# Performance work log

Hardware: AMD Instinct MI355X
Metric: run time of the kernel (lower is better)

Reference implementation:

```python
import jax, jax.numpy as jnp
import numpy as np
import math

B, S, H = 8, 1024, 768
NH = 12
DH = H // NH


def _linear(x, W, b):
    # torch Linear: y = x @ W.T + b, W: [out, in]
    return jnp.einsum('bsd,ed->bse', x, W) + b


def _split_heads(x):
    # [B,S,H] -> [B,NH,S,DH]
    b, s, _ = x.shape
    return x.reshape(b, s, NH, DH).transpose(0, 2, 1, 3)


def _attend(q, k, v):
    # q,k,v: [B,NH,S,DH]
    scores = jnp.einsum('bhqd,bhkd->bhqk', q, k) / math.sqrt(DH)
    probs = jax.nn.softmax(scores, axis=-1)
    ctx = jnp.einsum('bhqk,bhkd->bhqd', probs, v)
    b, h, s, d = ctx.shape
    return ctx.transpose(0, 2, 1, 3).reshape(b, s, h * d)


def setup_inputs() -> dict:
    key = jax.random.key(0)
    ks = jax.random.split(key, 20)
    sc = 1.0 / math.sqrt(H)
    inp = {
        'hidden_statesx': jax.random.normal(ks[0], (B, S, H), jnp.float32),
        'hidden_statesy': jax.random.normal(ks[1], (B, S, H), jnp.float32),
    }
    names = ['Wq', 'Wk', 'Wv', 'Wo', 'Wqd', 'Wkd', 'Wvd', 'Wod']
    for i, n in enumerate(names):
        inp[n] = jax.random.normal(ks[2 + i], (H, H), jnp.float32) * sc
        inp['b' + n[1:]] = jnp.zeros((H,), jnp.float32)
    inp['w11'] = jnp.full((1,), 0.5, jnp.float32)
    inp['w12'] = jnp.full((1,), 0.5, jnp.float32)
    inp['w21'] = jnp.full((1,), 0.5, jnp.float32)
    inp['w22'] = jnp.full((1,), 0.5, jnp.float32)
    return inp


def reference(hidden_statesx, hidden_statesy,
              Wq, bq, Wk, bk, Wv, bv, Wo, bo,
              Wqd, bqd, Wkd, bkd, Wvd, bvd, Wod, bod,
              w11, w12, w21, w22):
    q = _split_heads(_linear(hidden_statesx, Wq, bq))
    k = _split_heads(_linear(hidden_statesx, Wk, bk))
    v = _split_heads(_linear(hidden_statesx, Wv, bv))
    qd = _split_heads(_linear(hidden_statesy, Wqd, bqd))
    kd = _split_heads(_linear(hidden_statesy, Wkd, bkd))
    vd = _split_heads(_linear(hidden_statesy, Wvd, bvd))

    # self-attention on x and y streams
    attention_sx = _linear(_attend(q, k, v), Wo, bo)
    attention_sy = _linear(_attend(qd, kd, vd), Wod, bod)
    # cross attentions (mba mode)
    attention_cx = _linear(_attend(q, kd, vd), Wo, bo)
    attention_cy = _linear(_attend(qd, k, v), Wod, bod)

    attention_sx = w11 * attention_sx + w12 * attention_cx
    attention_sy = w21 * attention_sy + w22 * attention_cy
    return attention_sx, attention_sy
```

## Files before the change

### kernel.cpp

```cpp
#include <hip/hip_runtime.h>

typedef __bf16 bf16;
typedef __bf16 bf16x8 __attribute__((ext_vector_type(8)));
typedef float f32x4 __attribute__((ext_vector_type(4)));

#define HD 768
#define ELTS 6291456
#define WELTS 589824

__device__ __forceinline__ void gld_lds16(const bf16* g, bf16* l) {
  __builtin_amdgcn_global_load_lds((const __attribute__((address_space(1))) void*)g,
                                   (__attribute__((address_space(3))) void*)l, 16, 0, 0);
}

__device__ __forceinline__ float rdscalar(const void* p, int f) {
  return f ? (float)((const bf16*)p)[0] : ((const float*)p)[0];
}

__device__ __forceinline__ float exp2fast(float x) {
#if __has_builtin(__builtin_amdgcn_exp2f)
  return __builtin_amdgcn_exp2f(x);
#else
  return __builtin_exp2f(x);
#endif
}

__global__ void probe_dtype(const unsigned int* __restrict__ x, int* flag) {
  const int t = threadIdx.x;
  int bad = 0;
#pragma unroll
  for (int i = 0; i < 4; ++i) {
    unsigned int wd = x[t * 4 + i];
    unsigned int e0 = (wd >> 7) & 0xFF;
    unsigned int e1 = (wd >> 23) & 0xFF;
    bad += (e0 >= 134) + (e1 >= 134);
  }
  unsigned long long m = __ballot(bad > 0);
  if (t == 0) *flag = (m == 0ULL) ? 1 : 0;
}

struct CvtArgs {
  const float* src[20];
  bf16* dst[20];
  int n[20];
  const int* flag;
};
__global__ __launch_bounds__(256) void convert_inputs(CvtArgs a) {
  if (*a.flag) return;
  const int seg = blockIdx.y;
  const float* s = a.src[seg];
  bf16* d = a.dst[seg];
  const int n4 = a.n[seg] >> 2;
  for (int i = blockIdx.x * blockDim.x + threadIdx.x; i < n4; i += gridDim.x * blockDim.x) {
    f32x4 v = *(const f32x4*)(s + i * 4);
    bf16 o[4];
#pragma unroll
    for (int e = 0; e < 4; ++e) o[e] = (bf16)v[e];
    *(unsigned long long*)(d + i * 4) = *(unsigned long long*)o;
  }
}

struct GemmArgs {
  const void* A[6];
  const void* Ac[6];
  const void* W[6];
  const void* Wc[6];
  const void* bias[6];
  const void* biasc[6];
  const void* s0[6];
  const void* s1[6];
  void* C[6];
  float cmul[6];
  int c_fixed[6];
  int vt[6];
  int ext_w[6];
  long long out_elem_off[6];
  const int* flag;
};

__global__ __launch_bounds__(256) void gemm_bt(GemmArgs args) {
  const int g = blockIdx.z;
  const int f = *args.flag;
  const bool c_bf = args.c_fixed[g] || f;
  const bool w_f32 = (!f) && args.ext_w[g];
  const bf16* __restrict__ A = (const bf16*)(f ? args.A[g] : args.Ac[g]);
  const void* __restrict__ Wp = f ? args.W[g] : args.Wc[g];
  const void* __restrict__ bias = f ? args.bias[g] : args.biasc[g];
  bf16* Cb = (bf16*)args.C[g] + args.out_elem_off[g];
  float* Cf = (float*)args.C[g] + args.out_elem_off[g];
  float bscale = 1.0f;
  if (args.s0[g]) bscale = rdscalar(args.s0[g], f) + rdscalar(args.s1[g], f);
  const float cmul = args.cmul[g];

  const int m0 = blockIdx.x * 128;
  const int n0 = blockIdx.y * 128;
  const int t = threadIdx.x;
  const int lane = t & 63;
  const int w = t >> 6;
  const int wm = (w >> 1) * 64, wn = (w & 1) * 64;

  __shared__ __attribute__((aligned(16))) bf16 As[128 * 64];
  __shared__ __attribute__((aligned(16))) bf16 Bs[128 * 64];

  f32x4 acc[4][4] = {};

  const int row_s = t >> 3, slot_s = t & 7;
  const int gswz = (slot_s ^ (row_s & 7)) << 3;

  const int fr = lane & 15;
  const int l4 = lane >> 4;
  const int sR0 = ((l4) ^ (fr & 7)) << 3;
  const int sR1 = ((4 + l4) ^ (fr & 7)) << 3;

  for (int kb = 0; kb < 12; ++kb) {
    const int k0 = kb * 64;
#pragma unroll
    for (int i = 0; i < 4; ++i) {
      const int row = row_s + i * 32;
      gld_lds16(A + (size_t)(m0 + row) * HD + k0 + gswz, As + (t + i * 256) * 8);
    }
    if (!w_f32) {
#pragma unroll
      for (int i = 0; i < 4; ++i) {
        const int row = row_s + i * 32;
        gld_lds16((const bf16*)Wp + (size_t)(n0 + row) * HD + k0 + gswz, Bs + (t + i * 256) * 8);
      }
    } else {
      const float* Wf = (const float*)Wp;
#pragma unroll
      for (int i = 0; i < 4; ++i) {
        const int row = row_s + i * 32;
        const size_t src = (size_t)(n0 + row) * HD + k0 + gswz;
        f32x4 u0 = *(const f32x4*)(Wf + src), u1 = *(const f32x4*)(Wf + src + 4);
        bf16x8 v;
#pragma unroll
        for (int e = 0; e < 4; ++e) { v[e] = (bf16)u0[e]; v[e + 4] = (bf16)u1[e]; }
        *(bf16x8*)(Bs + (t + i * 256) * 8) = v;
      }
    }
    __syncthreads();
#pragma unroll
    for (int kk = 0; kk < 2; ++kk) {
      const int sR = kk ? sR1 : sR0;
      bf16x8 af[4], bfr[4];
#pragma unroll
      for (int mi = 0; mi < 4; ++mi)
        af[mi] = *(const bf16x8*)(As + (wm + mi * 16 + fr) * 64 + sR);
#pragma unroll
      for (int ni = 0; ni < 4; ++ni)
        bfr[ni] = *(const bf16x8*)(Bs + (wn + ni * 16 + fr) * 64 + sR);
#pragma unroll
      for (int mi = 0; mi < 4; ++mi)
#pragma unroll
        for (int ni = 0; ni < 4; ++ni)
          acc[mi][ni] = __builtin_amdgcn_mfma_f32_16x16x32_bf16(af[mi], bfr[ni], acc[mi][ni], 0, 0, 0);
    }
    __syncthreads();
  }

  const int rq = (lane >> 4) * 4;
  const int is_vt = args.vt[g];
#pragma unroll
  for (int ni = 0; ni < 4; ++ni) {
    const int col = n0 + wn + ni * 16 + fr;
    const float bv = (w_f32 ? ((const float*)bias)[col]
                            : (float)((const bf16*)bias)[col]) * bscale;
#pragma unroll
    for (int mi = 0; mi < 4; ++mi) {
      const int row = m0 + wm + mi * 16 + rq;
      if (is_vt) {
        const int bb = row >> 10, s = row & 1023;
        const int hh = col >> 6, d = col & 63;
        bf16 tmp[4];
#pragma unroll
        for (int r = 0; r < 4; ++r) tmp[r] = (bf16)((acc[mi][ni][r] + bv) * cmul);
        *(unsigned long long*)(Cb + (((size_t)(bb * 12 + hh)) << 16) + (d << 10) + s) =
            *(const unsigned long long*)tmp;
      } else {
#pragma unroll
        for (int r = 0; r < 4; ++r) {
          const float val = (acc[mi][ni][r] + bv) * cmul;
          if (c_bf) Cb[(size_t)(row + r) * HD + col] = (bf16)val;
          else      Cf[(size_t)(row + r) * HD + col] = val;
        }
      }
    }
  }
}

__global__ __launch_bounds__(256, 2) void attn_mba(
    const bf16* __restrict__ Q, const bf16* __restrict__ Kx, const bf16* __restrict__ Vtx,
    const bf16* __restrict__ Qd, const bf16* __restrict__ Kd, const bf16* __restrict__ Vtd,
    const void* w11, const void* w12, const void* w21, const void* w22,
    bf16* ctxX, bf16* ctxY, const int* flag) {
  const int linear = blockIdx.x + (blockIdx.y << 4);
  const int swz = (linear & 7) * 192 + (linear >> 3);
  const int qb = swz & 15;
  const int bh = swz >> 4;
  const int b = bh / 12;
  const int f = *flag;

  const float wgtX[2] = {rdscalar(w11, f), rdscalar(w12, f)};
  const float wgtY[2] = {rdscalar(w22, f), rdscalar(w21, f)};

  const size_t tok0 = (size_t)b * 1024;
  const size_t vbase = (size_t)bh * 65536;
  const int fcol = (bh - b * 12) * 64;
  const int q0 = qb * 64;

  __shared__ __attribute__((aligned(16))) bf16 smem[16384];
  bf16* Ks = smem;
  bf16* Vs = smem + 8192;

  const int t = threadIdx.x, lane = t & 63, w = t >> 6;
  const int l15 = lane & 15, l4 = lane >> 4;

  const int g0 = t >> 3, slot0 = t & 7;
  const int g1 = g0 + 32;
  const int gs = (slot0 ^ (g0 & 7)) << 3;
  const int kp0 = (g0 & 32) + ((g0 & 12) << 1) + ((g0 & 16) >> 2) + (g0 & 3);
  const int kp1 = (g1 & 32) + ((g1 & 12) << 1) + ((g1 & 16) >> 2) + (g1 & 3);
  const size_t koffg0 = (tok0 + kp0) * HD + fcol + gs;
  const size_t koffg1 = (tok0 + kp1) * HD + fcol + gs;
  const size_t voffg0 = vbase + (size_t)g0 * 1024 + gs;
  const size_t voffg1 = vbase + (size_t)g1 * 1024 + gs;

  auto stage = [&](int nit) {
    const bf16* Kc = nit < 16 ? Kx : Kd;
    const bf16* Vc = nit < 16 ? Vtx : Vtd;
    const int kt64 = (nit & 15) * 64;
    bf16* Kb = Ks + (nit & 1) * 4096;
    bf16* Vb = Vs + (nit & 1) * 4096;
    gld_lds16(Kc + koffg0 + (size_t)kt64 * HD, Kb + t * 8);
    gld_lds16(Kc + koffg1 + (size_t)kt64 * HD, Kb + (t + 256) * 8);
    gld_lds16(Vc + voffg0 + kt64, Vb + t * 8);
    gld_lds16(Vc + voffg1 + kt64, Vb + (t + 256) * 8);
  };

  stage(0);

  const int qrow = w * 16 + l15;
  const bf16* qp0 = Q  + (tok0 + q0 + qrow) * HD + fcol;
  const bf16* qp1 = Qd + (tok0 + q0 + qrow) * HD + fcol;
  bf16x8 qf[2][2];
  qf[0][0] = *(const bf16x8*)(qp0 + (l4 << 3));
  qf[0][1] = *(const bf16x8*)(qp0 + ((4 + l4) << 3));
  qf[1][0] = *(const bf16x8*)(qp1 + (l4 << 3));
  qf[1][1] = *(const bf16x8*)(qp1 + ((4 + l4) << 3));

  const int kbase = l15 * 64 + ((l4 ^ (l15 & 7)) << 3);

  __syncthreads();

  f32x4 mixX[4] = {}, mixY[4] = {};
  f32x4 oacc[2][4] = {};
  f32x4 lsum[2] = {};

  for (int it = 0; it < 32; ++it) {
    if (it) __syncthreads();
    if (it + 1 < 32) stage(it + 1);
    const bf16* Kb = Ks + (it & 1) * 4096;
    const bf16* Vb = Vs + (it & 1) * 4096;

    const bf16* vpa = Vb + kbase;
    const bf16* vpb = Vb + (kbase ^ 32);
    const bf16x8 va0 = *(const bf16x8*)(vpa);
    const bf16x8 va1 = *(const bf16x8*)(vpa + 1024);
    const bf16x8 va2 = *(const bf16x8*)(vpa + 2048);
    const bf16x8 va3 = *(const bf16x8*)(vpa + 3072);
    const bf16x8 vb0 = *(const bf16x8*)(vpb);
    const bf16x8 vb1 = *(const bf16x8*)(vpb + 1024);
    const bf16x8 vb2 = *(const bf16x8*)(vpb + 2048);
    const bf16x8 vb3 = *(const bf16x8*)(vpb + 3072);

    f32x4 sv0[4], sv1[4];
    __builtin_amdgcn_s_setprio(1);
#pragma unroll
    for (int mi = 0; mi < 4; ++mi) {
      const bf16x8 kf0 = *(const bf16x8*)(Kb + (kbase + mi * 1024));
      const bf16x8 kf1 = *(const bf16x8*)(Kb + ((kbase ^ 32) + mi * 1024));
      f32x4 a = {}, c = {};
      a = __builtin_amdgcn_mfma_f32_16x16x32_bf16(kf0, qf[0][0], a, 0, 0, 0);
      c = __builtin_amdgcn_mfma_f32_16x16x32_bf16(kf0, qf[1][0], c, 0, 0, 0);
      a = __builtin_amdgcn_mfma_f32_16x16x32_bf16(kf1, qf[0][1], a, 0, 0, 0);
      c = __builtin_amdgcn_mfma_f32_16x16x32_bf16(kf1, qf[1][1], c, 0, 0, 0);
      sv0[mi] = a; sv1[mi] = c;
    }
    __builtin_amdgcn_s_setprio(0);

    bf16x8 pf00, pf01;
    {
      f32x4 ls = lsum[0];
#pragma unroll
      for (int mi = 0; mi < 4; ++mi) {
        f32x4 e;
#pragma unroll
        for (int r = 0; r < 4; ++r) e[r] = exp2fast(sv0[mi][r]);
        sv0[mi] = e;
        ls += e;
      }
      lsum[0] = ls;
#pragma unroll
      for (int j = 0; j < 8; ++j) {
        pf00[j] = (bf16)sv0[(j >> 2)][j & 3];
        pf01[j] = (bf16)sv0[2 + (j >> 2)][j & 3];
      }
    }
    bf16x8 pf10, pf11;
    {
      f32x4 ls = lsum[1];
#pragma unroll
      for (int mi = 0; mi < 4; ++mi) {
        f32x4 e;
#pragma unroll
        for (int r = 0; r < 4; ++r) e[r] = exp2fast(sv1[mi][r]);
        sv1[mi] = e;
        ls += e;
      }
      lsum[1] = ls;
#pragma unroll
      for (int j = 0; j < 8; ++j) {
        pf10[j] = (bf16)sv1[(j >> 2)][j & 3];
        pf11[j] = (bf16)sv1[2 + (j >> 2)][j & 3];
      }
    }

    __builtin_amdgcn_s_setprio(1);
    oacc[0][0] = __builtin_amdgcn_mfma_f32_16x16x32_bf16(va0, pf00, oacc[0][0], 0, 0, 0);
    oacc[1][0] = __builtin_amdgcn_mfma_f32_16x16x32_bf16(va0, pf10, oacc[1][0], 0, 0, 0);
    oacc[0][1] = __builtin_amdgcn_mfma_f32_16x16x32_bf16(va1, pf00, oacc[0][1], 0, 0, 0);
    oacc[1][1] = __builtin_amdgcn_mfma_f32_16x16x32_bf16(va1, pf10, oacc[1][1], 0, 0, 0);
    oacc[0][2] = __builtin_amdgcn_mfma_f32_16x16x32_bf16(va2, pf00, oacc[0][2], 0, 0, 0);
    oacc[1][2] = __builtin_amdgcn_mfma_f32_16x16x32_bf16(va2, pf10, oacc[1][2], 0, 0, 0);
    oacc[0][3] = __builtin_amdgcn_mfma_f32_16x16x32_bf16(va3, pf00, oacc[0][3], 0, 0, 0);
    oacc[1][3] = __builtin_amdgcn_mfma_f32_16x16x32_bf16(va3, pf10, oacc[1][3], 0, 0, 0);
    oacc[0][0] = __builtin_amdgcn_mfma_f32_16x16x32_bf16(vb0, pf01, oacc[0][0], 0, 0, 0);
    oacc[1][0] = __builtin_amdgcn_mfma_f32_16x16x32_bf16(vb0, pf11, oacc[1][0], 0, 0, 0);
    oacc[0][1] = __builtin_amdgcn_mfma_f32_16x16x32_bf16(vb1, pf01, oacc[0][1], 0, 0, 0);
    oacc[1][1] = __builtin_amdgcn_mfma_f32_16x16x32_bf16(vb1, pf11, oacc[1][1], 0, 0, 0);
    oacc[0][2] = __builtin_amdgcn_mfma_f32_16x16x32_bf16(vb2, pf01, oacc[0][2], 0, 0, 0);
    oacc[1][2] = __builtin_amdgcn_mfma_f32_16x16x32_bf16(vb2, pf11, oacc[1][2], 0, 0, 0);
    oacc[0][3] = __builtin_amdgcn_mfma_f32_16x16x32_bf16(vb3, pf01, oacc[0][3], 0, 0, 0);
    oacc[1][3] = __builtin_amdgcn_mfma_f32_16x16x32_bf16(vb3, pf11, oacc[1][3], 0, 0, 0);
    __builtin_amdgcn_s_setprio(0);

    if ((it & 15) == 15) {
      const int ph = it >> 4;
      float l0 = (lsum[0][0] + lsum[0][1]) + (lsum[0][2] + lsum[0][3]);
      float l1 = (lsum[1][0] + lsum[1][1]) + (lsum[1][2] + lsum[1][3]);
      l0 += __shfl_xor(l0, 16); l0 += __shfl_xor(l0, 32);
      l1 += __shfl_xor(l1, 16); l1 += __shfl_xor(l1, 32);
      const float scX = wgtX[ph] / l0;
      const float scY = wgtY[ph] / l1;
#pragma unroll
      for (int mi = 0; mi < 4; ++mi) {
#pragma unroll
        for (int r = 0; r < 4; ++r) {
          mixX[mi][r] += scX * oacc[0][mi][r];
          mixY[mi][r] += scY * oacc[1][mi][r];
        }
        oacc[0][mi] = f32x4{};
        oacc[1][mi] = f32x4{};
      }
      lsum[0] = f32x4{};
      lsum[1] = f32x4{};
    }
  }

  __syncthreads();
  bf16* TX = smem;
  bf16* TY = smem + 4608;
#pragma unroll
  for (int mi = 0; mi < 4; ++mi)
#pragma unroll
    for (int r = 0; r < 4; ++r) {
      TX[qrow * 72 + mi * 16 + l4 * 4 + r] = (bf16)mixX[mi][r];
      TY[qrow * 72 + mi * 16 + l4 * 4 + r] = (bf16)mixY[mi][r];
    }
  __syncthreads();
#pragma unroll
  for (int i = 0; i < 2; ++i) {
    const int q = t + i * 256;
    const int g = q >> 3, dc = (q & 7) * 8;
    *(bf16x8*)(ctxX + (tok0 + q0 + g) * HD + fcol + dc) = *(const bf16x8*)(TX + g * 72 + dc);
    *(bf16x8*)(ctxY + (tok0 + q0 + g) * HD + fcol + dc) = *(const bf16x8*)(TY + g * 72 + dc);
  }
}

extern "C" void kernel_launch(void* const* d_in, const int* in_sizes, int n_in,
                              void* d_out, int out_size, void* d_ws, size_t ws_size,
                              hipStream_t stream) {
  (void)in_sizes; (void)n_in; (void)out_size;
  const void* x = d_in[0];
  const void* y = d_in[1];

  bf16* ws = (bf16*)d_ws;
  bf16* Qb   = ws + 0ull * ELTS;
  bf16* Kb   = ws + 1ull * ELTS;
  bf16* Vtb  = ws + 2ull * ELTS;
  bf16* Qdb  = ws + 3ull * ELTS;
  bf16* Kdb  = ws + 4ull * ELTS;
  bf16* Vtdb = ws + 5ull * ELTS;
  bf16* ctxX = Qb;
  bf16* ctxY = Qdb;
  int* flag = (int*)(ws + 6ull * ELTS);

  const size_t extra_elems = 6ull * ELTS + 32 + 2ull * WELTS + 2 * 768;
  const bool big_ws = ws_size >= extra_elems * sizeof(bf16);
  bf16* extraW = ws + 6ull * ELTS + 32;
  bf16* extraB = extraW + 2ull * WELTS;

  bf16* cb = (bf16*)d_out;
  bf16* xb = cb;
  bf16* yb = cb + (size_t)ELTS;
  bf16* Wcv = cb + 2ull * ELTS;
  bf16* bcv = Wcv + 6ull * WELTS;

  probe_dtype<<<dim3(1), dim3(64), 0, stream>>>((const unsigned int*)x, flag);

  CvtArgs ca;
  int nseg = 14;
  {
    const int wsrc[6] = {2, 4, 6, 10, 12, 14};
    ca.src[0] = (const float*)x;  ca.dst[0] = xb;  ca.n[0] = ELTS;
    ca.src[1] = (const float*)y;  ca.dst[1] = yb;  ca.n[1] = ELTS;
    for (int i = 0; i < 6; ++i) {
      ca.src[2 + i] = (const float*)d_in[wsrc[i]];
      ca.dst[2 + i] = Wcv + (size_t)i * WELTS;
      ca.n[2 + i] = WELTS;
      ca.src[8 + i] = (const float*)d_in[wsrc[i] + 1];
      ca.dst[8 + i] = bcv + (size_t)i * 768;
      ca.n[8 + i] = 768;
    }
    if (big_ws) {
      ca.src[14] = (const float*)d_in[8];  ca.dst[14] = extraW;         ca.n[14] = WELTS;
      ca.src[15] = (const float*)d_in[16]; ca.dst[15] = extraW + WELTS; ca.n[15] = WELTS;
      ca.src[16] = (const float*)d_in[9];  ca.dst[16] = extraB;         ca.n[16] = 768;
      ca.src[17] = (const float*)d_in[17]; ca.dst[17] = extraB + 768;   ca.n[17] = 768;
      nseg = 18;
    }
    ca.flag = flag;
  }
  convert_inputs<<<dim3(512, nseg), dim3(256), 0, stream>>>(ca);

  GemmArgs gq;
  {
    const void* A6[6]  = {x, x, x, y, y, y};
    const void* Ac6[6] = {xb, xb, xb, yb, yb, yb};
    const int di[6] = {2, 4, 6, 10, 12, 14};
    bf16* C6[6] = {Qb, Kb, Vtb, Qdb, Kdb, Vtdb};
    for (int i = 0; i < 6; ++i) {
      gq.A[i] = A6[i]; gq.Ac[i] = Ac6[i];
      gq.W[i] = d_in[di[i]]; gq.Wc[i] = Wcv + (size_t)i * WELTS;
      gq.bias[i] = d_in[di[i] + 1]; gq.biasc[i] = bcv + (size_t)i * 768;
      gq.s0[i] = nullptr; gq.s1[i] = nullptr; gq.C[i] = C6[i];
      gq.cmul[i] = (i == 0 || i == 3) ? 0.18033688011112042f : 1.0f;
      gq.c_fixed[i] = 1; gq.ext_w[i] = 0; gq.out_elem_off[i] = 0;
      gq.vt[i] = (i == 2 || i == 5) ? 1 : 0;
    }
    gq.flag = flag;
  }
  gemm_bt<<<dim3(64, 6, 6), dim3(256), 0, stream>>>(gq);

  attn_mba<<<dim3(16, 96), dim3(256), 0, stream>>>(
      Qb, Kb, Vtb, Qdb, Kdb, Vtdb, d_in[18], d_in[19], d_in[20], d_in[21],
      ctxX, ctxY, flag);

  GemmArgs gp;
  for (int i = 0; i < 6; ++i) {
    gp.A[i] = ctxX; gp.Ac[i] = ctxX;
    gp.W[i] = d_in[8]; gp.Wc[i] = d_in[8];
    gp.bias[i] = d_in[9]; gp.biasc[i] = d_in[9];
    gp.s0[i] = d_in[18]; gp.s1[i] = d_in[19]; gp.C[i] = d_out;
    gp.cmul[i] = 1.0f; gp.c_fixed[i] = 0; gp.vt[i] = 0;
    gp.ext_w[i] = 1; gp.out_elem_off[i] = 0;
  }
  gp.A[1] = ctxY; gp.Ac[1] = ctxY;
  gp.W[1] = d_in[16]; gp.Wc[1] = d_in[16];
  gp.bias[1] = d_in[17]; gp.biasc[1] = d_in[17];
  gp.s0[1] = d_in[20]; gp.s1[1] = d_in[21];
  gp.out_elem_off[1] = (long long)ELTS;
  if (big_ws) {
    gp.Wc[0] = extraW;         gp.biasc[0] = extraB;       gp.ext_w[0] = 0;
    gp.Wc[1] = extraW + WELTS; gp.biasc[1] = extraB + 768; gp.ext_w[1] = 0;
  }
  gp.flag = flag;
  gemm_bt<<<dim3(64, 6, 2), dim3(256), 0, stream>>>(gp);
}
```

Measured before the change: 372.0 us.

## Double-buffer GEMM LDS tiles with K=32 to overlap loads and MFMA

Splits the projection GEMM's 64-wide K tile into two 32-wide LDS buffers and prefetches the next tile while MFMAs run on the current one. The swizzle is adapted to 4 slots per row. The goal is to hide global-to-LDS load latency behind compute while keeping total LDS use the same. In exchange there are twice as many K iterations, each with fewer MFMAs per barrier, so sync overhead relative to compute goes up.

```diff
diff --git a/kernel.cpp b/kernel.cpp
--- a/kernel.cpp
+++ b/kernel.cpp
@@ -99,63 +99,61 @@
   const int w = t >> 6;
   const int wm = (w >> 1) * 64, wn = (w & 1) * 64;
 
-  __shared__ __attribute__((aligned(16))) bf16 As[128 * 64];
-  __shared__ __attribute__((aligned(16))) bf16 Bs[128 * 64];
+  __shared__ __attribute__((aligned(16))) bf16 As[2][128 * 32];
+  __shared__ __attribute__((aligned(16))) bf16 Bs[2][128 * 32];
 
   f32x4 acc[4][4] = {};
 
-  const int row_s = t >> 3, slot_s = t & 7;
-  const int gswz = (slot_s ^ (row_s & 7)) << 3;
+  const int row_s = t >> 2;
+  const int gswz = (((t & 3) ^ (row_s & 3)) << 3);
 
   const int fr = lane & 15;
   const int l4 = lane >> 4;
-  const int sR0 = ((l4) ^ (fr & 7)) << 3;
-  const int sR1 = ((4 + l4) ^ (fr & 7)) << 3;
-
-  for (int kb = 0; kb < 12; ++kb) {
-    const int k0 = kb * 64;
-#pragma unroll
-    for (int i = 0; i < 4; ++i) {
-      const int row = row_s + i * 32;
-      gld_lds16(A + (size_t)(m0 + row) * HD + k0 + gswz, As + (t + i * 256) * 8);
-    }
+  const int sR = ((l4 ^ (fr & 3)) << 3);
+
+  auto stageAB = [&](int kb) {
+    const int buf = kb & 1;
+    const int k0 = kb * 32;
+    gld_lds16(A + (size_t)(m0 + row_s) * HD + k0 + gswz, &As[buf][t * 8]);
+    gld_lds16(A + (size_t)(m0 + row_s + 64) * HD + k0 + gswz, &As[buf][(t + 256) * 8]);
     if (!w_f32) {
-#pragma unroll
-      for (int i = 0; i < 4; ++i) {
-        const int row = row_s + i * 32;
-        gld_lds16((const bf16*)Wp + (size_t)(n0 + row) * HD + k0 + gswz, Bs + (t + i * 256) * 8);
-      }
+      gld_lds16((const bf16*)Wp + (size_t)(n0 + row_s) * HD + k0 + gswz, &Bs[buf][t * 8]);
+      gld_lds16((const bf16*)Wp + (size_t)(n0 + row_s + 64) * HD + k0 + gswz, &Bs[buf][(t + 256) * 8]);
     } else {
       const float* Wf = (const float*)Wp;
 #pragma unroll
-      for (int i = 0; i < 4; ++i) {
-        const int row = row_s + i * 32;
+      for (int i = 0; i < 2; ++i) {
+        const int row = row_s + i * 64;
         const size_t src = (size_t)(n0 + row) * HD + k0 + gswz;
         f32x4 u0 = *(const f32x4*)(Wf + src), u1 = *(const f32x4*)(Wf + src + 4);
         bf16x8 v;
 #pragma unroll
         for (int e = 0; e < 4; ++e) { v[e] = (bf16)u0[e]; v[e + 4] = (bf16)u1[e]; }
-        *(bf16x8*)(Bs + (t + i * 256) * 8) = v;
-      }
-    }
-    __syncthreads();
-#pragma unroll
-    for (int kk = 0; kk < 2; ++kk) {
-      const int sR = kk ? sR1 : sR0;
-      bf16x8 af[4], bfr[4];
-#pragma unroll
-      for (int mi = 0; mi < 4; ++mi)
-        af[mi] = *(const bf16x8*)(As + (wm + mi * 16 + fr) * 64 + sR);
+        *(bf16x8*)(&Bs[buf][(t + i * 256) * 8]) = v;
+      }
+    }
+  };
+
+  stageAB(0);
+  __syncthreads();
+
+  for (int kb = 0; kb < 24; ++kb) {
+    if (kb) __syncthreads();
+    if (kb + 1 < 24) stageAB(kb + 1);
+    const bf16* Ab = As[kb & 1];
+    const bf16* Bb = Bs[kb & 1];
+    bf16x8 af[4], bfr[4];
+#pragma unroll
+    for (int mi = 0; mi < 4; ++mi)
+      af[mi] = *(const bf16x8*)(Ab + (wm + mi * 16 + fr) * 32 + sR);
+#pragma unroll
+    for (int ni = 0; ni < 4; ++ni)
+      bfr[ni] = *(const bf16x8*)(Bb + (wn + ni * 16 + fr) * 32 + sR);
+#pragma unroll
+    for (int mi = 0; mi < 4; ++mi)
 #pragma unroll
       for (int ni = 0; ni < 4; ++ni)
-        bfr[ni] = *(const bf16x8*)(Bs + (wn + ni * 16 + fr) * 64 + sR);
-#pragma unroll
-      for (int mi = 0; mi < 4; ++mi)
-#pragma unroll
-        for (int ni = 0; ni < 4; ++ni)
-          acc[mi][ni] = __builtin_amdgcn_mfma_f32_16x16x32_bf16(af[mi], bfr[ni], acc[mi][ni], 0, 0, 0);
-    }
-    __syncthreads();
+        acc[mi][ni] = __builtin_amdgcn_mfma_f32_16x16x32_bf16(af[mi], bfr[ni], acc[mi][ni], 0, 0, 0);
   }
 
   const int rq = (lane >> 4) * 4;
```

Result: no change. 369.5 us (-0.7%).
